# Kernel tuning notes

Hardware: AMD Instinct MI355X
Metric: run time of the kernel (lower is better)

## Reference

```python
import jax, jax.numpy as jnp
import numpy as np


def setup_inputs() -> dict:
    key = jax.random.key(0)
    x = jax.random.normal(key, (64, 512, 16, 16), dtype=jnp.float32)
    return {"x": x}


def reference(x):
    # x: [B, dim, h, w] -> covariance pooling y: [B, dim, dim]
    B, dim, h, w = x.shape
    M = h * w
    xf = x.reshape(B, dim, M)
    # I_hat = (1/M) I - (1/M^2) 11^T  (centering matrix scaled by 1/M)
    inv_M = jnp.asarray(1.0 / M, dtype=x.dtype)
    I_hat = inv_M * jnp.eye(M, dtype=x.dtype) - (inv_M * inv_M) * jnp.ones((M, M), dtype=x.dtype)
    # y = x @ I_hat @ x^T, I_hat broadcast over batch
    xI = jnp.einsum('bdm,mn->bdn', xf, I_hat)   # [B, dim, M]
    y = jnp.einsum('bdn,ben->bde', xI, xf)      # [B, dim, dim]
    return y
```

## Files before the change

### kernel.cpp

```cpp
#include <hip/hip_runtime.h>
#include <stdint.h>


typedef __attribute__((ext_vector_type(8))) short bf16x8;
typedef __attribute__((ext_vector_type(4))) float f32x4;

static __device__ __forceinline__ unsigned short f2bf(float f) {
    union { float f; uint32_t u; } c; c.f = f;
    uint32_t u = c.u;
    return (unsigned short)((u + 0x7FFFu + ((u >> 16) & 1u)) >> 16);
}

static __device__ __forceinline__ void cvt_store(f32x4 v0, f32x4 v1, float* psum,
                                                 unsigned short* dst) {
    v0 *= 0.0625f; v1 *= 0.0625f;
    *psum += (v0.x + v0.y + v0.z + v0.w) + (v1.x + v1.y + v1.z + v1.w);
    bf16x8 o;
    o[0] = (short)f2bf(v0.x); o[1] = (short)f2bf(v0.y);
    o[2] = (short)f2bf(v0.z); o[3] = (short)f2bf(v0.w);
    o[4] = (short)f2bf(v1.x); o[5] = (short)f2bf(v1.y);
    o[6] = (short)f2bf(v1.z); o[7] = (short)f2bf(v1.w);
    *(bf16x8*)dst = o;
}

__global__ __launch_bounds__(256) void covpool_fused(const float* __restrict__ x,
                                                     float* __restrict__ y) {
    __shared__ __align__(16) unsigned short As[128 * 32];
    __shared__ __align__(16) unsigned short Bs[128 * 32];
    __shared__ __align__(16) float Ep[32 * 132];
    __shared__ float muA[128];
    __shared__ float muB[128];

    const int xcd = blockIdx.x & 7;
    const int j   = blockIdx.x >> 3;
    const int b   = xcd * 8 + j / 10;
    const int t10 = j % 10;
    const unsigned code = (unsigned)((0xFBA7653210ULL >> (4 * t10)) & 15ULL);
    const int tm = code >> 2, tn = code & 3;
    const bool diag = (tm == tn);

    const float* Ag = x + ((size_t)b * 512 + tm * 128) * 256;
    const float* Bg = x + ((size_t)b * 512 + tn * 128) * 256;

    const int tid  = threadIdx.x;
    const int lane = tid & 63;
    const int wave = tid >> 6;
    const int wm = (wave >> 1) * 64;
    const int wn = (wave & 1) * 64;

    f32x4 acc[4][4] = {};
    float pA[2] = {0.f, 0.f}, pB[2] = {0.f, 0.f};

    const int rl  = lane & 15;
    const int q   = lane >> 4;
    const int swl = (q ^ ((rl >> 1) & 3)) * 8;
    const int srow = tid >> 2, schunk = tid & 3;

    f32x4 a0[2], a1[2], b0[2], b1[2];
#pragma unroll
    for (int t = 0; t < 2; ++t) {
        const float* g = Ag + (size_t)(t * 64 + srow) * 256 + schunk * 8;
        a0[t] = *(const f32x4*)g; a1[t] = *(const f32x4*)(g + 4);
        if (!diag) {
            const float* h = Bg + (size_t)(t * 64 + srow) * 256 + schunk * 8;
            b0[t] = *(const f32x4*)h; b1[t] = *(const f32x4*)(h + 4);
        }
    }

    for (int kk = 0; kk < 256; kk += 32) {
        __syncthreads();
#pragma unroll
        for (int t = 0; t < 2; ++t) {
            const int row  = t * 64 + srow;
            const int slot = schunk ^ ((row >> 1) & 3);
            cvt_store(a0[t], a1[t], &pA[t], As + row * 32 + slot * 8);
            if (!diag) cvt_store(b0[t], b1[t], &pB[t], Bs + row * 32 + slot * 8);
        }
        __syncthreads();
        if (kk < 224) {
#pragma unroll
            for (int t = 0; t < 2; ++t) {
                const float* g = Ag + (size_t)(t * 64 + srow) * 256 + (kk + 32) + schunk * 8;
                a0[t] = *(const f32x4*)g; a1[t] = *(const f32x4*)(g + 4);
                if (!diag) {
                    const float* h = Bg + (size_t)(t * 64 + srow) * 256 + (kk + 32) + schunk * 8;
                    b0[t] = *(const f32x4*)h; b1[t] = *(const f32x4*)(h + 4);
                }
            }
        }
        const unsigned short* Bsrc = diag ? As : Bs;
        bf16x8 af[4], bfr[4];
#pragma unroll
        for (int i = 0; i < 4; ++i)
            af[i] = *(const bf16x8*)(As + (wm + i * 16 + rl) * 32 + swl);
#pragma unroll
        for (int jj = 0; jj < 4; ++jj)
            bfr[jj] = *(const bf16x8*)(Bsrc + (wn + jj * 16 + rl) * 32 + swl);
#pragma unroll
        for (int i = 0; i < 4; ++i)
#pragma unroll
            for (int jj = 0; jj < 4; ++jj)
                acc[i][jj] = __builtin_amdgcn_mfma_f32_16x16x32_bf16(
                    af[i], bfr[jj], acc[i][jj], 0, 0, 0);
    }

#pragma unroll
    for (int t = 0; t < 2; ++t) {
        float s = pA[t];
        s += __shfl_xor(s, 1, 64); s += __shfl_xor(s, 2, 64);
        if (schunk == 0) muA[t * 64 + srow] = s * 0.0625f;
        if (!diag) {
            float sb = pB[t];
            sb += __shfl_xor(sb, 1, 64); sb += __shfl_xor(sb, 2, 64);
            if (schunk == 0) muB[t * 64 + srow] = sb * 0.0625f;
        }
    }
    const float* muBp = diag ? muA : muB;
    float* yb = y + (size_t)b * 512 * 512;

#pragma unroll
    for (int c = 0; c < 4; ++c) {
        __syncthreads();
        if ((wave >> 1) == (c >> 1)) {
            const int ii0 = 2 * (c & 1);
#pragma unroll
            for (int ii = 0; ii < 2; ++ii) {
                const int i = ii0 + ii;
#pragma unroll
                for (int jj = 0; jj < 4; ++jj) {
                    const int col = wn + jj * 16 + rl;
                    const float mb = muBp[col];
#pragma unroll
                    for (int r = 0; r < 4; ++r) {
                        const int row = wm + i * 16 + q * 4 + r;
                        Ep[(ii * 16 + q * 4 + r) * 132 + col] = acc[i][jj][r] - muA[row] * mb;
                    }
                }
            }
        }
        __syncthreads();
#pragma unroll
        for (int v = 0; v < 4; ++v) {
            const int flat = v * 256 + tid;
            const int rloc = flat >> 5, c4 = flat & 31;
            f32x4 val = *(const f32x4*)(Ep + rloc * 132 + c4 * 4);
            *(f32x4*)(yb + (size_t)(tm * 128 + c * 32 + rloc) * 512 + tn * 128 + c4 * 4) = val;
        }
        if (!diag) {
#pragma unroll
            for (int v = 0; v < 4; ++v) {
                const int id = v * 256 + tid;
                const int cc = id >> 3, g = id & 7;
                f32x4 val;
#pragma unroll
                for (int e = 0; e < 4; ++e)
                    val[e] = Ep[(g * 4 + e) * 132 + cc];
                *(f32x4*)(yb + (size_t)(tn * 128 + cc) * 512 + tm * 128 + c * 32 + g * 4) = val;
            }
        }
    }
}

extern "C" void kernel_launch(void* const* d_in, const int* in_sizes, int n_in,
                              void* d_out, int out_size, void* d_ws, size_t ws_size,
                              hipStream_t stream) {
    const float* x = (const float*)d_in[0];
    float* yout = (float*)d_out;
    (void)d_ws; (void)ws_size;
    covpool_fused<<<640, 256, 0, stream>>>(x, yout);
}
```

Baseline: 101.8 us.

## Shrink output tiles to 64x64 over upper-triangular tiles for more blocks

Each block now computes a 64x64 tile instead of 128x128. The grid covers the 36 upper-triangular tiles per batch, giving 2304 blocks instead of 640, with a smaller 2x2 MFMA accumulator per wave and a single-pass epilogue. The staging buffer is aliased with the bf16 operand tiles in shared memory, and launch bounds request 4 blocks per CU to raise occupancy and parallelism. The cost is more redundant global reads of input rows across tiles. The padded epilogue stride of 67 floats also means some 16-byte LDS reads are not naturally aligned.

```diff
diff --git a/kernel.cpp b/kernel.cpp
--- a/kernel.cpp
+++ b/kernel.cpp
@@ -23,140 +23,126 @@
     *(bf16x8*)dst = o;
 }
 
-__global__ __launch_bounds__(256) void covpool_fused(const float* __restrict__ x,
-                                                     float* __restrict__ y) {
-    __shared__ __align__(16) unsigned short As[128 * 32];
-    __shared__ __align__(16) unsigned short Bs[128 * 32];
-    __shared__ __align__(16) float Ep[32 * 132];
-    __shared__ float muA[128];
-    __shared__ float muB[128];
+__global__ __launch_bounds__(256, 4) void covpool_fused(const float* __restrict__ x,
+                                                        float* __restrict__ y) {
+    __shared__ __align__(16) char smem[64 * 67 * 4];
+    unsigned short* As = (unsigned short*)smem;
+    unsigned short* Bs = (unsigned short*)(smem + 4096);
+    float* Ep = (float*)smem;
+    __shared__ float muA[64];
+    __shared__ float muB[64];
 
     const int xcd = blockIdx.x & 7;
     const int j   = blockIdx.x >> 3;
-    const int b   = xcd * 8 + j / 10;
-    const int t10 = j % 10;
-    const unsigned code = (unsigned)((0xFBA7653210ULL >> (4 * t10)) & 15ULL);
-    const int tm = code >> 2, tn = code & 3;
+    const int b   = xcd * 8 + j / 36;
+    int t = j % 36;
+    int tm = 0;
+    while (t >= 8 - tm) { t -= (8 - tm); ++tm; }
+    const int tn = tm + t;
     const bool diag = (tm == tn);
 
-    const float* Ag = x + ((size_t)b * 512 + tm * 128) * 256;
-    const float* Bg = x + ((size_t)b * 512 + tn * 128) * 256;
+    const float* Ag = x + ((size_t)b * 512 + tm * 64) * 256;
+    const float* Bg = x + ((size_t)b * 512 + tn * 64) * 256;
 
     const int tid  = threadIdx.x;
     const int lane = tid & 63;
     const int wave = tid >> 6;
-    const int wm = (wave >> 1) * 64;
-    const int wn = (wave & 1) * 64;
+    const int wm = (wave >> 1) * 32;
+    const int wn = (wave & 1) * 32;
 
-    f32x4 acc[4][4] = {};
-    float pA[2] = {0.f, 0.f}, pB[2] = {0.f, 0.f};
+    f32x4 acc[2][2] = {};
+    float pA = 0.f, pB = 0.f;
 
     const int rl  = lane & 15;
     const int q   = lane >> 4;
     const int swl = (q ^ ((rl >> 1) & 3)) * 8;
     const int srow = tid >> 2, schunk = tid & 3;
+    const int sslot = schunk ^ ((srow >> 1) & 3);
 
-    f32x4 a0[2], a1[2], b0[2], b1[2];
-#pragma unroll
-    for (int t = 0; t < 2; ++t) {
-        const float* g = Ag + (size_t)(t * 64 + srow) * 256 + schunk * 8;
-        a0[t] = *(const f32x4*)g; a1[t] = *(const f32x4*)(g + 4);
+    f32x4 a0, a1, b0, b1;
+    {
+        const float* g = Ag + (size_t)srow * 256 + schunk * 8;
+        a0 = *(const f32x4*)g; a1 = *(const f32x4*)(g + 4);
         if (!diag) {
-            const float* h = Bg + (size_t)(t * 64 + srow) * 256 + schunk * 8;
-            b0[t] = *(const f32x4*)h; b1[t] = *(const f32x4*)(h + 4);
+            const float* h = Bg + (size_t)srow * 256 + schunk * 8;
+            b0 = *(const f32x4*)h; b1 = *(const f32x4*)(h + 4);
         }
     }
 
     for (int kk = 0; kk < 256; kk += 32) {
         __syncthreads();
-#pragma unroll
-        for (int t = 0; t < 2; ++t) {
-            const int row  = t * 64 + srow;
-            const int slot = schunk ^ ((row >> 1) & 3);
-            cvt_store(a0[t], a1[t], &pA[t], As + row * 32 + slot * 8);
-            if (!diag) cvt_store(b0[t], b1[t], &pB[t], Bs + row * 32 + slot * 8);
-        }
+        cvt_store(a0, a1, &pA, As + srow * 32 + sslot * 8);
+        if (!diag) cvt_store(b0, b1, &pB, Bs + srow * 32 + sslot * 8);
         __syncthreads();
         if (kk < 224) {
-#pragma unroll
-            for (int t = 0; t < 2; ++t) {
-                const float* g = Ag + (size_t)(t * 64 + srow) * 256 + (kk + 32) + schunk * 8;
-                a0[t] = *(const f32x4*)g; a1[t] = *(const f32x4*)(g + 4);
-                if (!diag) {
-                    const float* h = Bg + (size_t)(t * 64 + srow) * 256 + (kk + 32) + schunk * 8;
-                    b0[t] = *(const f32x4*)h; b1[t] = *(const f32x4*)(h + 4);
-                }
+            const float* g = Ag + (size_t)srow * 256 + (kk + 32) + schunk * 8;
+            a0 = *(const f32x4*)g; a1 = *(const f32x4*)(g + 4);
+            if (!diag) {
+                const float* h = Bg + (size_t)srow * 256 + (kk + 32) + schunk * 8;
+                b0 = *(const f32x4*)h; b1 = *(const f32x4*)(h + 4);
             }
         }
         const unsigned short* Bsrc = diag ? As : Bs;
-        bf16x8 af[4], bfr[4];
+        bf16x8 af[2], bfr[2];
 #pragma unroll
-        for (int i = 0; i < 4; ++i)
+        for (int i = 0; i < 2; ++i)
             af[i] = *(const bf16x8*)(As + (wm + i * 16 + rl) * 32 + swl);
 #pragma unroll
-        for (int jj = 0; jj < 4; ++jj)
+        for (int jj = 0; jj < 2; ++jj)
             bfr[jj] = *(const bf16x8*)(Bsrc + (wn + jj * 16 + rl) * 32 + swl);
 #pragma unroll
-        for (int i = 0; i < 4; ++i)
+        for (int i = 0; i < 2; ++i)
 #pragma unroll
-            for (int jj = 0; jj < 4; ++jj)
+            for (int jj = 0; jj < 2; ++jj)
                 acc[i][jj] = __builtin_amdgcn_mfma_f32_16x16x32_bf16(
                     af[i], bfr[jj], acc[i][jj], 0, 0, 0);
     }
 
-#pragma unroll
-    for (int t = 0; t < 2; ++t) {
-        float s = pA[t];
+    {
+        float s = pA;
         s += __shfl_xor(s, 1, 64); s += __shfl_xor(s, 2, 64);
-        if (schunk == 0) muA[t * 64 + srow] = s * 0.0625f;
+        if (schunk == 0) muA[srow] = s * 0.0625f;
         if (!diag) {
-            float sb = pB[t];
+            float sb = pB;
             sb += __shfl_xor(sb, 1, 64); sb += __shfl_xor(sb, 2, 64);
-            if (schunk == 0) muB[t * 64 + srow] = sb * 0.0625f;
+            if (schunk == 0) muB[srow] = sb * 0.0625f;
         }
     }
+    __syncthreads();
+
     const float* muBp = diag ? muA : muB;
-    float* yb = y + (size_t)b * 512 * 512;
-
 #pragma unroll
-    for (int c = 0; c < 4; ++c) {
-        __syncthreads();
-        if ((wave >> 1) == (c >> 1)) {
-            const int ii0 = 2 * (c & 1);
+    for (int i = 0; i < 2; ++i)
 #pragma unroll
-            for (int ii = 0; ii < 2; ++ii) {
-                const int i = ii0 + ii;
+        for (int jj = 0; jj < 2; ++jj) {
+            const int col = wn + jj * 16 + rl;
+            const float mb = muBp[col];
 #pragma unroll
-                for (int jj = 0; jj < 4; ++jj) {
-                    const int col = wn + jj * 16 + rl;
-                    const float mb = muBp[col];
-#pragma unroll
-                    for (int r = 0; r < 4; ++r) {
-                        const int row = wm + i * 16 + q * 4 + r;
-                        Ep[(ii * 16 + q * 4 + r) * 132 + col] = acc[i][jj][r] - muA[row] * mb;
-                    }
-                }
+            for (int r = 0; r < 4; ++r) {
+                const int row = wm + i * 16 + q * 4 + r;
+                Ep[row * 67 + col] = acc[i][jj][r] - muA[row] * mb;
             }
         }
-        __syncthreads();
+    __syncthreads();
+
+    float* yb = y + (size_t)b * 512 * 512;
+#pragma unroll
+    for (int v = 0; v < 4; ++v) {
+        const int flat = v * 256 + tid;
+        const int row = flat >> 4, c4 = flat & 15;
+        f32x4 val = *(const f32x4*)(Ep + row * 67 + c4 * 4);
+        *(f32x4*)(yb + (size_t)(tm * 64 + row) * 512 + tn * 64 + c4 * 4) = val;
+    }
+    if (!diag) {
 #pragma unroll
         for (int v = 0; v < 4; ++v) {
-            const int flat = v * 256 + tid;
-            const int rloc = flat >> 5, c4 = flat & 31;
-            f32x4 val = *(const f32x4*)(Ep + rloc * 132 + c4 * 4);
-            *(f32x4*)(yb + (size_t)(tm * 128 + c * 32 + rloc) * 512 + tn * 128 + c4 * 4) = val;
-        }
-        if (!diag) {
+            const int id = v * 256 + tid;
+            const int cc = id >> 4, g = id & 15;
+            f32x4 val;
 #pragma unroll
-            for (int v = 0; v < 4; ++v) {
-                const int id = v * 256 + tid;
-                const int cc = id >> 3, g = id & 7;
-                f32x4 val;
-#pragma unroll
-                for (int e = 0; e < 4; ++e)
-                    val[e] = Ep[(g * 4 + e) * 132 + cc];
-                *(f32x4*)(yb + (size_t)(tn * 128 + cc) * 512 + tm * 128 + c * 32 + g * 4) = val;
-            }
+            for (int e = 0; e < 4; ++e)
+                val[e] = Ep[(g * 4 + e) * 67 + cc];
+            *(f32x4*)(yb + (size_t)(tn * 64 + cc) * 512 + tm * 64 + g * 4) = val;
         }
     }
 }
@@ -167,5 +153,5 @@
     const float* x = (const float*)d_in[0];
     float* yout = (float*)d_out;
     (void)d_ws; (void)ws_size;
-    covpool_fused<<<640, 256, 0, stream>>>(x, yout);
+    covpool_fused<<<2304, 256, 0, stream>>>(x, yout);
 }
```

New measurement: 106.7 us. +4.8%, slower.
